# Kernel tuning notes

Measured on AMD Instinct MI355X. Metric: run time of the kernel, lower is better.

## Reference

```python
import jax, jax.numpy as jnp
import numpy as np

B, T, D, H, OUT = 1024, 512, 6, 128, 8


def setup_inputs() -> dict:
    key = jax.random.key(0)
    ks = jax.random.split(key, 24)
    n = lambda k, shp, s=0.05: jax.random.normal(k, shp, dtype=jnp.float32) * s
    return {
        "src": jax.random.normal(ks[0], (B, T, D), dtype=jnp.float32),
        # pointwise conv stack (kernel size 1 -> plain matmuls)
        "w0": n(ks[1], (H, D)), "b0": n(ks[2], (H,)),
        "w1": n(ks[3], (H, H)), "b1": n(ks[4], (H,)),
        "w2": n(ks[5], (H, H)), "b2": n(ks[6], (H,)),
        "w3": n(ks[7], (H, H)), "b3": n(ks[8], (H,)),
        "pos_embed": n(ks[9], (T, 1, H)),
        # LSTM layer 0 (PyTorch gate order i,f,g,o stacked along dim 0)
        "Wih0": n(ks[10], (4 * H, H)), "Whh0": n(ks[11], (4 * H, H)),
        "bih0": n(ks[12], (4 * H,)), "bhh0": n(ks[13], (4 * H,)),
        # LSTM layer 1
        "Wih1": n(ks[14], (4 * H, H)), "Whh1": n(ks[15], (4 * H, H)),
        "bih1": n(ks[16], (4 * H,)), "bhh1": n(ks[17], (4 * H,)),
        # head: LayerNorm + Linear(H, H//4) + GELU + Linear(H//4, OUT)
        "ln_g": jnp.ones((H,), jnp.float32), "ln_b": jnp.zeros((H,), jnp.float32),
        "hw1": n(ks[18], (H // 4, H)), "hb1": n(ks[19], (H // 4,)),
        "hw2": n(ks[20], (OUT, H // 4)), "hb2": n(ks[21], (OUT,)),
    }


def _gelu(x):
    return jax.nn.gelu(x, approximate=False)  # torch default GELU (erf)


def _lstm_layer(xs, Wih, Whh, bih, bhh):
    # xs: (T, B, H) time-major; returns (all hidden states, final hidden state)
    Hd = Whh.shape[1]
    Bd = xs.shape[1]
    bias = bih + bhh
    h0 = jnp.zeros((Bd, Hd), xs.dtype)
    c0 = jnp.zeros((Bd, Hd), xs.dtype)

    def step(carry, x):
        h, c = carry
        z = x @ Wih.T + h @ Whh.T + bias  # (B, 4H)
        i, f, g, o = jnp.split(z, 4, axis=-1)
        c = jax.nn.sigmoid(f) * c + jax.nn.sigmoid(i) * jnp.tanh(g)
        h = jax.nn.sigmoid(o) * jnp.tanh(c)
        return (h, c), h

    (h, _), ys = jax.lax.scan(step, (h0, c0), xs)
    return ys, h


def reference(src, w0, b0, w1, b1, w2, b2, w3, b3, pos_embed,
              Wih0, Whh0, bih0, bhh0, Wih1, Whh1, bih1, bhh1,
              ln_g, ln_b, hw1, hb1, hw2, hb2):
    # pointwise Conv1d+GELU stack (kernel=1 -> per-timestep matmul), eval mode
    x = _gelu(src @ w0.T + b0)            # (B, T, H)
    x = _gelu(x @ w1.T + b1)
    x = _gelu(x @ w2.T + b2)
    x = _gelu(x @ w3.T + b3)
    x = jnp.transpose(x, (1, 0, 2)) + pos_embed  # (T, B, H), broadcast pos over batch
    ys, _ = _lstm_layer(x, Wih0, Whh0, bih0, bhh0)
    _, h = _lstm_layer(ys, Wih1, Whh1, bih1, bhh1)  # final hidden of last layer, (B, H)
    # head: LayerNorm (eps=1e-5) -> Linear -> GELU -> Linear (dropout inactive in eval)
    mu = h.mean(-1, keepdims=True)
    var = ((h - mu) ** 2).mean(-1, keepdims=True)
    hn = (h - mu) * jax.lax.rsqrt(var + 1e-5) * ln_g + ln_b
    return _gelu(hn @ hw1.T + hb1) @ hw2.T + hb2  # (B, OUT)
```

## Files before the change

kernel.cpp:

```cpp
#include <hip/hip_runtime.h>
#include <hip/hip_bf16.h>
#include <cstdint>

#define T_ 512
#define B_ 1024
#define D_ 6
#define H_ 128
#define CH_ 8
#define CT_ 16

typedef _Float16 f16;
typedef _Float16 f16x8 __attribute__((ext_vector_type(8)));
typedef float f32x4 __attribute__((ext_vector_type(4)));

__device__ __forceinline__ float erf_f(float x) {
    float ax = fabsf(x);
    float t = __builtin_amdgcn_rcpf(fmaf(0.3275911f, ax, 1.f));
    float p = fmaf(t, 1.061405429f, -1.453152027f);
    p = fmaf(t, p, 1.421413741f);
    p = fmaf(t, p, -0.284496736f);
    p = fmaf(t, p, 0.254829592f);
    p = p * t;
    float e = __builtin_amdgcn_exp2f(-ax * ax * 1.4426950408889634f);
    float r = 1.f - p * e;
    return copysignf(r, x);
}
__device__ __forceinline__ float gelu_f(float x) {
    return 0.5f * x * (1.f + erf_f(x * 0.7071067811865476f));
}
__device__ __forceinline__ float sig_f(float x) {
    return __builtin_amdgcn_rcpf(1.f + __builtin_amdgcn_exp2f(-1.4426950408889634f * x));
}
__device__ __forceinline__ float tanh_f(float x) {
    return 2.f * sig_f(2.f * x) - 1.f;
}
__device__ __forceinline__ f16x8 load8cvt(const float* p) {
    float4 a = ((const float4*)p)[0];
    float4 b = ((const float4*)p)[1];
    f16x8 r = { (f16)a.x, (f16)a.y, (f16)a.z, (f16)a.w,
                (f16)b.x, (f16)b.y, (f16)b.z, (f16)b.w };
    return r;
}
__device__ __forceinline__ f16x8 lds_rd8(const f16* base, int row, int cb) {
    const char* p = (const char*)base + row * 256 + (cb ^ ((row & 7) << 4));
    return *(const f16x8*)p;
}
__device__ __forceinline__ void lds_wr1(f16* base, int row, int col, f16 v) {
    char* p = (char*)base + row * 256 + ((col * 2) ^ ((row & 7) << 4));
    *(f16*)p = v;
}
__device__ __forceinline__ void zx_wr(f16* base, int row, int col, f16 v) {
    char* p = (char*)base + row * 1024 + ((col * 2) ^ ((row & 7) << 4));
    *(f16*)p = v;
}
__device__ __forceinline__ float zx_rd(const f16* base, int row, int col) {
    const char* p = (const char*)base + row * 1024 + ((col * 2) ^ ((row & 7) << 4));
    return (float)*(const f16*)p;
}

__global__ __launch_bounds__(512) void conv_k(
    const float* __restrict__ src,
    const float* __restrict__ w0p, const float* __restrict__ b0p,
    const float* __restrict__ w1p, const float* __restrict__ b1p,
    const float* __restrict__ w2p, const float* __restrict__ b2p,
    const float* __restrict__ w3p, const float* __restrict__ b3p,
    const float* __restrict__ posp, f16* __restrict__ xout)
{
    __shared__ f16 XA0[64 * 128];
    __shared__ f16 XA1[64 * 128];
    const int tid = threadIdx.x;
    const int lane = tid & 63, wid = tid >> 6;
    const int l16 = lane & 15, hi = lane >> 4;
    const int t0 = (blockIdx.x & 31) * CT_;
    const int bb0 = (blockIdx.x >> 5) * 4;
    const int mycol = wid * 16 + l16;

    f16x8 cw[3][4];
    {
        const float* wp[3] = { w1p, w2p, w3p };
#pragma unroll
        for (int L = 0; L < 3; ++L)
#pragma unroll
            for (int ki = 0; ki < 4; ++ki)
                cw[L][ki] = load8cvt(wp[L] + mycol * 128 + ki * 32 + hi * 8);
    }
    const int col0 = tid & 127;
    const int r0 = tid >> 7;
    float w0c[6], b0c;
#pragma unroll
    for (int k = 0; k < 6; ++k) w0c[k] = w0p[col0 * 6 + k];
    b0c = b0p[col0];
    const float b1c = b1p[mycol], b2c = b2p[mycol], b3c = b3p[mycol];

    {
        const float2* sp0 = (const float2*)src + ((size_t)(bb0 + r0) * T_ + t0) * 3;
#pragma unroll
        for (int it = 0; it < CT_; ++it) {
            float2 a = sp0[it * 3 + 0], b = sp0[it * 3 + 1], c2 = sp0[it * 3 + 2];
            float acc = b0c;
            acc = fmaf(a.x, w0c[0], acc);
            acc = fmaf(a.y, w0c[1], acc);
            acc = fmaf(b.x, w0c[2], acc);
            acc = fmaf(b.y, w0c[3], acc);
            acc = fmaf(c2.x, w0c[4], acc);
            acc = fmaf(c2.y, w0c[5], acc);
            lds_wr1(XA0, it * 4 + r0, col0, (f16)gelu_f(acc));
        }
    }
    __syncthreads();

    auto conv_mfma = [&](const f16* Xin, f16* Xout, int L, float bc, bool addpos) {
#pragma unroll
        for (int mt = 0; mt < 4; ++mt) {
            f16x8 af[4];
#pragma unroll
            for (int ki = 0; ki < 4; ++ki)
                af[ki] = lds_rd8(Xin, mt * 16 + l16, ki * 64 + hi * 16);
            f32x4 acc = { bc, bc, bc, bc };
#pragma unroll
            for (int ki = 0; ki < 4; ++ki)
                acc = __builtin_amdgcn_mfma_f32_16x16x32_f16(af[ki], cw[L][ki], acc, 0, 0, 0);
            float pv = 0.f;
            if (addpos) pv = posp[(t0 + mt * 4 + hi) * 128 + mycol];
#pragma unroll
            for (int j = 0; j < 4; ++j)
                lds_wr1(Xout, mt * 16 + hi * 4 + j, mycol, (f16)(gelu_f(acc[j]) + pv));
        }
    };
    conv_mfma(XA0, XA1, 0, b1c, false);
    __syncthreads();
    conv_mfma(XA1, XA0, 1, b2c, false);
    __syncthreads();
    conv_mfma(XA0, XA1, 2, b3c, true);
    __syncthreads();

#pragma unroll
    for (int pass = 0; pass < 2; ++pass) {
        int u = pass * 512 + tid;
        int tau = u >> 4, cw8 = u & 15;
        f16x8 v = lds_rd8(XA1, tau, cw8 * 16);
        *(f16x8*)(xout + (size_t)(t0 + (tau >> 2)) * (B_ * H_) +
                  (size_t)(bb0 + (tau & 3)) * H_ + cw8 * 8) = v;
    }
}

template <bool WRITE_YS, bool WRITE_H>
__global__ __launch_bounds__(512) void lstm_chunk_k(
    const f16* __restrict__ xb,
    const float* __restrict__ Wih, const float* __restrict__ Whh,
    const float* __restrict__ bih, const float* __restrict__ bhh,
    f16* __restrict__ ys, float* __restrict__ hfin)
{
    __shared__ f16 ZX[32 * 512];
    __shared__ f16 YH[32 * 128];
    __shared__ f16 HL[2][4 * 128];

    const int tid = threadIdx.x;
    const int lane = tid & 63, wid = tid >> 6;
    const int l16 = lane & 15, hi = lane >> 4;
    const int bb0 = blockIdx.x * 4;
    const int mycol = wid * 16 + l16;

    f16x8 whh[4][4];
    float biasg[4];
#pragma unroll
    for (int g = 0; g < 4; ++g) {
        int n = g * 128 + mycol;
        biasg[g] = bih[n] + bhh[n];
#pragma unroll
        for (int ki = 0; ki < 4; ++ki)
            whh[g][ki] = load8cvt(Whh + n * 128 + ki * 32 + hi * 8);
    }
    for (int i = tid; i < 2 * 4 * 128; i += 512) ((f16*)HL)[i] = (f16)0.f;

    float c = 0.f, h = 0.f;
    __syncthreads();

    auto flushYH = [&](int tc) {
        int tau = tid >> 4, cw8 = tid & 15;
        f16x8 v = lds_rd8(YH, tau, cw8 * 16);
        *(f16x8*)(ys + (size_t)(tc + (tau >> 2)) * (B_ * H_) +
                  (size_t)(bb0 + (tau & 3)) * H_ + cw8 * 8) = v;
    };

    for (int t0 = 0; t0 < T_; t0 += CH_) {
        if (WRITE_YS && t0 > 0) flushYH(t0 - CH_);
        {
            f16x8 af[2][4];
#pragma unroll
            for (int mt = 0; mt < 2; ++mt) {
                const int tau = mt * 16 + l16;
                const f16* ap = xb + (size_t)(t0 + (tau >> 2)) * (B_ * H_) +
                                (size_t)(bb0 + (tau & 3)) * H_;
#pragma unroll
                for (int ki = 0; ki < 4; ++ki)
                    af[mt][ki] = *(const f16x8*)(ap + ki * 32 + hi * 8);
            }
#pragma unroll
            for (int nt = 0; nt < 4; ++nt) {
                const int n = wid * 64 + nt * 16 + l16;
                f16x8 bf[4];
#pragma unroll
                for (int ki = 0; ki < 4; ++ki)
                    bf[ki] = load8cvt(Wih + n * 128 + ki * 32 + hi * 8);
                f32x4 za0 = { 0.f, 0.f, 0.f, 0.f };
                f32x4 za1 = { 0.f, 0.f, 0.f, 0.f };
#pragma unroll
                for (int ki = 0; ki < 4; ++ki) {
                    za0 = __builtin_amdgcn_mfma_f32_16x16x32_f16(af[0][ki], bf[ki], za0, 0, 0, 0);
                    za1 = __builtin_amdgcn_mfma_f32_16x16x32_f16(af[1][ki], bf[ki], za1, 0, 0, 0);
                }
#pragma unroll
                for (int j = 0; j < 4; ++j) {
                    zx_wr(ZX, hi * 4 + j, wid * 64 + nt * 16 + l16, (f16)za0[j]);
                    zx_wr(ZX, 16 + hi * 4 + j, wid * 64 + nt * 16 + l16, (f16)za1[j]);
                }
                __builtin_amdgcn_sched_barrier(0);
            }
        }
        __syncthreads();
        for (int it = 0; it < CH_; ++it) {
            const int t = t0 + it;
            f16x8 ha[4];
#pragma unroll
            for (int ki = 0; ki < 4; ++ki)
                ha[ki] = lds_rd8(HL[t & 1], l16 >> 2, ki * 64 + hi * 16);
            f32x4 acc[4];
#pragma unroll
            for (int g = 0; g < 4; ++g) {
                f32x4 bv = { biasg[g], biasg[g], biasg[g], biasg[g] };
                acc[g] = bv;
            }
#pragma unroll
            for (int ki = 0; ki < 4; ++ki)
#pragma unroll
                for (int g = 0; g < 4; ++g)
                    acc[g] = __builtin_amdgcn_mfma_f32_16x16x32_f16(ha[ki], whh[g][ki], acc[g], 0, 0, 0);
            float zi = acc[0][0] + zx_rd(ZX, it * 4 + hi, 0 + mycol);
            float zf = acc[1][0] + zx_rd(ZX, it * 4 + hi, 128 + mycol);
            float zg = acc[2][0] + zx_rd(ZX, it * 4 + hi, 256 + mycol);
            float zo = acc[3][0] + zx_rd(ZX, it * 4 + hi, 384 + mycol);
            c = sig_f(zf) * c + sig_f(zi) * tanh_f(zg);
            h = sig_f(zo) * tanh_f(c);
            lds_wr1(HL[(t + 1) & 1], hi, mycol, (f16)h);
            if (WRITE_YS) lds_wr1(YH, it * 4 + hi, mycol, (f16)h);
            __syncthreads();
        }
    }
    if (WRITE_YS) flushYH(T_ - CH_);
    if (WRITE_H) hfin[(size_t)(bb0 + hi) * H_ + mycol] = h;
}

__global__ __launch_bounds__(256) void head_k(
    const float* __restrict__ hfin,
    const float* __restrict__ lng, const float* __restrict__ lnb,
    const float* __restrict__ hw1, const float* __restrict__ hb1,
    const float* __restrict__ hw2, const float* __restrict__ hb2,
    float* __restrict__ outp)
{
    __shared__ float HN[4][128];
    __shared__ float G[4][32];
    const int tid = threadIdx.x, lane = tid & 63, wid = tid >> 6;
    const int b = blockIdx.x * 4 + wid;
    float v0 = hfin[b * 128 + lane], v1 = hfin[b * 128 + 64 + lane];
    float s = v0 + v1;
#pragma unroll
    for (int m = 1; m < 64; m <<= 1) s += __shfl_xor(s, m);
    float mu = s * (1.f / 128.f);
    float d0 = v0 - mu, d1 = v1 - mu;
    float q = d0 * d0 + d1 * d1;
#pragma unroll
    for (int m = 1; m < 64; m <<= 1) q += __shfl_xor(q, m);
    float rs = rsqrtf(q * (1.f / 128.f) + 1e-5f);
    HN[wid][lane] = d0 * rs * lng[lane] + lnb[lane];
    HN[wid][64 + lane] = d1 * rs * lng[64 + lane] + lnb[64 + lane];
    __syncthreads();
    if (tid < 128) {
        int row = tid >> 5, o = tid & 31;
        float a = hb1[o];
#pragma unroll 4
        for (int k = 0; k < 128; ++k) a = fmaf(HN[row][k], hw1[o * 128 + k], a);
        G[row][o] = gelu_f(a);
    }
    __syncthreads();
    if (tid < 32) {
        int row = tid >> 3, oo = tid & 7;
        float a = hb2[oo];
#pragma unroll
        for (int k = 0; k < 32; ++k) a = fmaf(G[row][k], hw2[oo * 32 + k], a);
        outp[(size_t)(blockIdx.x * 4 + row) * 8 + oo] = a;
    }
}

extern "C" void kernel_launch(void* const* d_in, const int* in_sizes, int n_in,
                              void* d_out, int out_size, void* d_ws, size_t ws_size,
                              hipStream_t stream) {
    (void)in_sizes; (void)n_in; (void)out_size; (void)ws_size;
    const float* src  = (const float*)d_in[0];
    const float* w0   = (const float*)d_in[1];
    const float* b0   = (const float*)d_in[2];
    const float* w1   = (const float*)d_in[3];
    const float* b1   = (const float*)d_in[4];
    const float* w2   = (const float*)d_in[5];
    const float* b2   = (const float*)d_in[6];
    const float* w3   = (const float*)d_in[7];
    const float* b3   = (const float*)d_in[8];
    const float* pos  = (const float*)d_in[9];
    const float* Wih0 = (const float*)d_in[10];
    const float* Whh0 = (const float*)d_in[11];
    const float* bih0 = (const float*)d_in[12];
    const float* bhh0 = (const float*)d_in[13];
    const float* Wih1 = (const float*)d_in[14];
    const float* Whh1 = (const float*)d_in[15];
    const float* bih1 = (const float*)d_in[16];
    const float* bhh1 = (const float*)d_in[17];
    const float* lng  = (const float*)d_in[18];
    const float* lnb  = (const float*)d_in[19];
    const float* hw1  = (const float*)d_in[20];
    const float* hb1  = (const float*)d_in[21];
    const float* hw2  = (const float*)d_in[22];
    const float* hb2  = (const float*)d_in[23];
    float* outp = (float*)d_out;

    f16* xbuf = (f16*)d_ws;
    float* hfin = (float*)((char*)d_ws + (size_t)134217728);

    conv_k<<<dim3(8192), dim3(512), 0, stream>>>(
        src, w0, b0, w1, b1, w2, b2, w3, b3, pos, xbuf);
    lstm_chunk_k<true, false><<<dim3(256), dim3(512), 0, stream>>>(
        xbuf, Wih0, Whh0, bih0, bhh0, xbuf, nullptr);
    lstm_chunk_k<false, true><<<dim3(256), dim3(512), 0, stream>>>(
        xbuf, Wih1, Whh1, bih1, bhh1, nullptr, hfin);
    head_k<<<dim3(256), dim3(256), 0, stream>>>(
        hfin, lng, lnb, hw1, hb1, hw2, hb2, outp);
}
```

Before: 1.063 ms.

## Fuse both LSTM layers into one producer-consumer kernel with chunk flags

Replaces the two sequential LSTM layer launches with a single 512-block launch. The first 256 blocks run layer 0 and publish each finished 8-step chunk of hidden states through a per-batch-group release flag. The other 256 blocks spin on that flag and run layer 1 on each chunk as it arrives, so the two layers overlap in time instead of running back to back. The cost is extra fences and polling. It also relies on all 512 blocks being resident at once, and it can deadlock if a consumer block is scheduled while its producer block is not.

```diff
diff --git a/kernel.cpp b/kernel.cpp
--- a/kernel.cpp
+++ b/kernel.cpp
@@ -8,6 +8,7 @@
 #define H_ 128
 #define CH_ 8
 #define CT_ 16
+#define NP_ 256
 
 typedef _Float16 f16;
 typedef _Float16 f16x8 __attribute__((ext_vector_type(8)));
@@ -144,12 +145,14 @@
     }
 }
 
-template <bool WRITE_YS, bool WRITE_H>
-__global__ __launch_bounds__(512) void lstm_chunk_k(
+__global__ __launch_bounds__(512) void lstm_pc_k(
     const f16* __restrict__ xb,
-    const float* __restrict__ Wih, const float* __restrict__ Whh,
-    const float* __restrict__ bih, const float* __restrict__ bhh,
-    f16* __restrict__ ys, float* __restrict__ hfin)
+    const float* __restrict__ Wih0, const float* __restrict__ Whh0,
+    const float* __restrict__ bih0, const float* __restrict__ bhh0,
+    const float* __restrict__ Wih1, const float* __restrict__ Whh1,
+    const float* __restrict__ bih1, const float* __restrict__ bhh1,
+    f16* __restrict__ ys, int* __restrict__ flags,
+    float* __restrict__ hfin)
 {
     __shared__ f16 ZX[32 * 512];
     __shared__ f16 YH[32 * 128];
@@ -158,8 +161,15 @@
     const int tid = threadIdx.x;
     const int lane = tid & 63, wid = tid >> 6;
     const int l16 = lane & 15, hi = lane >> 4;
-    const int bb0 = blockIdx.x * 4;
+    const bool producer = (int)blockIdx.x < NP_;
+    const int p = producer ? (int)blockIdx.x : (int)blockIdx.x - NP_;
+    const int bb0 = p * 4;
     const int mycol = wid * 16 + l16;
+
+    const float* Wih = producer ? Wih0 : Wih1;
+    const float* Whh = producer ? Whh0 : Whh1;
+    const float* bih = producer ? bih0 : bih1;
+    const float* bhh = producer ? bhh0 : bhh1;
 
     f16x8 whh[4][4];
     float biasg[4];
@@ -176,49 +186,41 @@
     float c = 0.f, h = 0.f;
     __syncthreads();
 
-    auto flushYH = [&](int tc) {
-        int tau = tid >> 4, cw8 = tid & 15;
-        f16x8 v = lds_rd8(YH, tau, cw8 * 16);
-        *(f16x8*)(ys + (size_t)(tc + (tau >> 2)) * (B_ * H_) +
-                  (size_t)(bb0 + (tau & 3)) * H_ + cw8 * 8) = v;
+    auto zgemm = [&](const f16* Asrc , int t0) {
+        f16x8 af[2][4];
+#pragma unroll
+        for (int mt = 0; mt < 2; ++mt) {
+            const int tau = mt * 16 + l16;
+            const f16* ap = Asrc + (size_t)(t0 + (tau >> 2)) * (B_ * H_) +
+                            (size_t)(bb0 + (tau & 3)) * H_;
+#pragma unroll
+            for (int ki = 0; ki < 4; ++ki)
+                af[mt][ki] = *(const f16x8*)(ap + ki * 32 + hi * 8);
+        }
+#pragma unroll
+        for (int nt = 0; nt < 4; ++nt) {
+            const int n = wid * 64 + nt * 16 + l16;
+            f16x8 bf[4];
+#pragma unroll
+            for (int ki = 0; ki < 4; ++ki)
+                bf[ki] = load8cvt(Wih + n * 128 + ki * 32 + hi * 8);
+            f32x4 za0 = { 0.f, 0.f, 0.f, 0.f };
+            f32x4 za1 = { 0.f, 0.f, 0.f, 0.f };
+#pragma unroll
+            for (int ki = 0; ki < 4; ++ki) {
+                za0 = __builtin_amdgcn_mfma_f32_16x16x32_f16(af[0][ki], bf[ki], za0, 0, 0, 0);
+                za1 = __builtin_amdgcn_mfma_f32_16x16x32_f16(af[1][ki], bf[ki], za1, 0, 0, 0);
+            }
+#pragma unroll
+            for (int j = 0; j < 4; ++j) {
+                zx_wr(ZX, hi * 4 + j, wid * 64 + nt * 16 + l16, (f16)za0[j]);
+                zx_wr(ZX, 16 + hi * 4 + j, wid * 64 + nt * 16 + l16, (f16)za1[j]);
+            }
+            __builtin_amdgcn_sched_barrier(0);
+        }
     };
 
-    for (int t0 = 0; t0 < T_; t0 += CH_) {
-        if (WRITE_YS && t0 > 0) flushYH(t0 - CH_);
-        {
-            f16x8 af[2][4];
-#pragma unroll
-            for (int mt = 0; mt < 2; ++mt) {
-                const int tau = mt * 16 + l16;
-                const f16* ap = xb + (size_t)(t0 + (tau >> 2)) * (B_ * H_) +
-                                (size_t)(bb0 + (tau & 3)) * H_;
-#pragma unroll
-                for (int ki = 0; ki < 4; ++ki)
-                    af[mt][ki] = *(const f16x8*)(ap + ki * 32 + hi * 8);
-            }
-#pragma unroll
-            for (int nt = 0; nt < 4; ++nt) {
-                const int n = wid * 64 + nt * 16 + l16;
-                f16x8 bf[4];
-#pragma unroll
-                for (int ki = 0; ki < 4; ++ki)
-                    bf[ki] = load8cvt(Wih + n * 128 + ki * 32 + hi * 8);
-                f32x4 za0 = { 0.f, 0.f, 0.f, 0.f };
-                f32x4 za1 = { 0.f, 0.f, 0.f, 0.f };
-#pragma unroll
-                for (int ki = 0; ki < 4; ++ki) {
-                    za0 = __builtin_amdgcn_mfma_f32_16x16x32_f16(af[0][ki], bf[ki], za0, 0, 0, 0);
-                    za1 = __builtin_amdgcn_mfma_f32_16x16x32_f16(af[1][ki], bf[ki], za1, 0, 0, 0);
-                }
-#pragma unroll
-                for (int j = 0; j < 4; ++j) {
-                    zx_wr(ZX, hi * 4 + j, wid * 64 + nt * 16 + l16, (f16)za0[j]);
-                    zx_wr(ZX, 16 + hi * 4 + j, wid * 64 + nt * 16 + l16, (f16)za1[j]);
-                }
-                __builtin_amdgcn_sched_barrier(0);
-            }
-        }
-        __syncthreads();
+    auto slots = [&](int t0, bool writeYH) {
         for (int it = 0; it < CH_; ++it) {
             const int t = t0 + it;
             f16x8 ha[4];
@@ -243,12 +245,44 @@
             c = sig_f(zf) * c + sig_f(zi) * tanh_f(zg);
             h = sig_f(zo) * tanh_f(c);
             lds_wr1(HL[(t + 1) & 1], hi, mycol, (f16)h);
-            if (WRITE_YS) lds_wr1(YH, it * 4 + hi, mycol, (f16)h);
-            __syncthreads();
-        }
-    }
-    if (WRITE_YS) flushYH(T_ - CH_);
-    if (WRITE_H) hfin[(size_t)(bb0 + hi) * H_ + mycol] = h;
+            if (writeYH) lds_wr1(YH, it * 4 + hi, mycol, (f16)h);
+            __syncthreads();
+        }
+    };
+
+    if (producer) {
+        for (int k = 0; k < T_ / CH_; ++k) {
+            const int t0 = k * CH_;
+            zgemm(xb, t0);
+            __syncthreads();
+            slots(t0, true);
+            {
+                int tau = tid >> 4, cw8 = tid & 15;
+                f16x8 v = lds_rd8(YH, tau, cw8 * 16);
+                *(f16x8*)(ys + (size_t)(t0 + (tau >> 2)) * (B_ * H_) +
+                          (size_t)(bb0 + (tau & 3)) * H_ + cw8 * 8) = v;
+            }
+            __threadfence();
+            __syncthreads();
+            if (tid == 0)
+                __hip_atomic_store(&flags[p], k + 1, __ATOMIC_RELEASE,
+                                   __HIP_MEMORY_SCOPE_AGENT);
+        }
+    } else {
+        for (int k = 0; k < T_ / CH_; ++k) {
+            const int t0 = k * CH_;
+            if (tid == 0) {
+                while (__hip_atomic_load(&flags[p], __ATOMIC_ACQUIRE,
+                                         __HIP_MEMORY_SCOPE_AGENT) < k + 1)
+                    __builtin_amdgcn_s_sleep(8);
+            }
+            __syncthreads();
+            zgemm(ys, t0);
+            __syncthreads();
+            slots(t0, false);
+        }
+        hfin[(size_t)(bb0 + hi) * H_ + mycol] = h;
+    }
 }
 
 __global__ __launch_bounds__(256) void head_k(
@@ -324,13 +358,14 @@
 
     f16* xbuf = (f16*)d_ws;
     float* hfin = (float*)((char*)d_ws + (size_t)134217728);
-
+    int* flags = (int*)((char*)d_ws + (size_t)134742016);
+
+    hipMemsetAsync(flags, 0, 1024, stream);
     conv_k<<<dim3(8192), dim3(512), 0, stream>>>(
         src, w0, b0, w1, b1, w2, b2, w3, b3, pos, xbuf);
-    lstm_chunk_k<true, false><<<dim3(256), dim3(512), 0, stream>>>(
-        xbuf, Wih0, Whh0, bih0, bhh0, xbuf, nullptr);
-    lstm_chunk_k<false, true><<<dim3(256), dim3(512), 0, stream>>>(
-        xbuf, Wih1, Whh1, bih1, bhh1, nullptr, hfin);
+    lstm_pc_k<<<dim3(512), dim3(512), 0, stream>>>(
+        xbuf, Wih0, Whh0, bih0, bhh0, Wih1, Whh1, bih1, bhh1,
+        xbuf , flags, hfin);
     head_k<<<dim3(256), dim3(256), 0, stream>>>(
         hfin, lng, lnb, hw1, hb1, hw2, hb2, outp);
 }
```

Measured after the change: 3.609 ms. 3.4x slower.

## Double LSTM time chunk and pre-convert input weights to fp16

Applied to the files above, without the earlier changes.

The LSTM input projection now covers 16 timesteps per chunk instead of 8, so each fp16 Wih tile loaded from global memory feeds four MFMA row tiles instead of two, and the per-chunk barrier and projection overhead is amortised over more steps. A new prep kernel converts Wih0/Wih1 to fp16 once per call, removing the repeated fp32 load and convert in the loop. The pointer is laundered so the weight loads are not hoisted. The ZX and YH shared buffers double in size, which raises LDS use and register pressure and may cut occupancy.

```diff
diff --git a/kernel.cpp b/kernel.cpp
--- a/kernel.cpp
+++ b/kernel.cpp
@@ -6,7 +6,7 @@
 #define B_ 1024
 #define D_ 6
 #define H_ 128
-#define CH_ 8
+#define CH_ 16
 #define CT_ 16
 
 typedef _Float16 f16;
@@ -41,6 +41,10 @@
                 (f16)b.x, (f16)b.y, (f16)b.z, (f16)b.w };
     return r;
 }
+__device__ __forceinline__ const f16* launder16(const f16* p) {
+    asm volatile("" : "+s"(p));
+    return p;
+}
 __device__ __forceinline__ f16x8 lds_rd8(const f16* base, int row, int cb) {
     const char* p = (const char*)base + row * 256 + (cb ^ ((row & 7) << 4));
     return *(const f16x8*)p;
@@ -56,6 +60,15 @@
 __device__ __forceinline__ float zx_rd(const f16* base, int row, int col) {
     const char* p = (const char*)base + row * 1024 + ((col * 2) ^ ((row & 7) << 4));
     return (float)*(const f16*)p;
+}
+
+__global__ __launch_bounds__(512) void prep_k(
+    const float* __restrict__ Wih0, const float* __restrict__ Wih1,
+    f16* __restrict__ w0f, f16* __restrict__ w1f)
+{
+    int i = blockIdx.x * 512 + threadIdx.x;
+    w0f[i] = (f16)Wih0[i];
+    w1f[i] = (f16)Wih1[i];
 }
 
 __global__ __launch_bounds__(512) void conv_k(
@@ -147,12 +160,12 @@
 template <bool WRITE_YS, bool WRITE_H>
 __global__ __launch_bounds__(512) void lstm_chunk_k(
     const f16* __restrict__ xb,
-    const float* __restrict__ Wih, const float* __restrict__ Whh,
+    const f16* __restrict__ Wihf, const float* __restrict__ Whh,
     const float* __restrict__ bih, const float* __restrict__ bhh,
     f16* __restrict__ ys, float* __restrict__ hfin)
 {
-    __shared__ f16 ZX[32 * 512];
-    __shared__ f16 YH[32 * 128];
+    __shared__ f16 ZX[64 * 512];
+    __shared__ f16 YH[64 * 128];
     __shared__ f16 HL[2][4 * 128];
 
     const int tid = threadIdx.x;
@@ -177,18 +190,22 @@
     __syncthreads();
 
     auto flushYH = [&](int tc) {
-        int tau = tid >> 4, cw8 = tid & 15;
-        f16x8 v = lds_rd8(YH, tau, cw8 * 16);
-        *(f16x8*)(ys + (size_t)(tc + (tau >> 2)) * (B_ * H_) +
-                  (size_t)(bb0 + (tau & 3)) * H_ + cw8 * 8) = v;
+#pragma unroll
+        for (int pass = 0; pass < 2; ++pass) {
+            int u = pass * 512 + tid;
+            int tau = u >> 4, cw8 = u & 15;
+            f16x8 v = lds_rd8(YH, tau, cw8 * 16);
+            *(f16x8*)(ys + (size_t)(tc + (tau >> 2)) * (B_ * H_) +
+                      (size_t)(bb0 + (tau & 3)) * H_ + cw8 * 8) = v;
+        }
     };
 
     for (int t0 = 0; t0 < T_; t0 += CH_) {
         if (WRITE_YS && t0 > 0) flushYH(t0 - CH_);
         {
-            f16x8 af[2][4];
-#pragma unroll
-            for (int mt = 0; mt < 2; ++mt) {
+            f16x8 af[4][4];
+#pragma unroll
+            for (int mt = 0; mt < 4; ++mt) {
                 const int tau = mt * 16 + l16;
                 const f16* ap = xb + (size_t)(t0 + (tau >> 2)) * (B_ * H_) +
                                 (size_t)(bb0 + (tau & 3)) * H_;
@@ -196,25 +213,31 @@
                 for (int ki = 0; ki < 4; ++ki)
                     af[mt][ki] = *(const f16x8*)(ap + ki * 32 + hi * 8);
             }
+            const f16* Wf = launder16(Wihf);
 #pragma unroll
             for (int nt = 0; nt < 4; ++nt) {
                 const int n = wid * 64 + nt * 16 + l16;
                 f16x8 bf[4];
 #pragma unroll
                 for (int ki = 0; ki < 4; ++ki)
-                    bf[ki] = load8cvt(Wih + n * 128 + ki * 32 + hi * 8);
-                f32x4 za0 = { 0.f, 0.f, 0.f, 0.f };
-                f32x4 za1 = { 0.f, 0.f, 0.f, 0.f };
-#pragma unroll
-                for (int ki = 0; ki < 4; ++ki) {
-                    za0 = __builtin_amdgcn_mfma_f32_16x16x32_f16(af[0][ki], bf[ki], za0, 0, 0, 0);
-                    za1 = __builtin_amdgcn_mfma_f32_16x16x32_f16(af[1][ki], bf[ki], za1, 0, 0, 0);
+                    bf[ki] = *(const f16x8*)(Wf + n * 128 + ki * 32 + hi * 8);
+                f32x4 za[4];
+#pragma unroll
+                for (int mt = 0; mt < 4; ++mt) {
+                    f32x4 zz = { 0.f, 0.f, 0.f, 0.f };
+                    za[mt] = zz;
                 }
 #pragma unroll
-                for (int j = 0; j < 4; ++j) {
-                    zx_wr(ZX, hi * 4 + j, wid * 64 + nt * 16 + l16, (f16)za0[j]);
-                    zx_wr(ZX, 16 + hi * 4 + j, wid * 64 + nt * 16 + l16, (f16)za1[j]);
-                }
+                for (int ki = 0; ki < 4; ++ki)
+#pragma unroll
+                    for (int mt = 0; mt < 4; ++mt)
+                        za[mt] = __builtin_amdgcn_mfma_f32_16x16x32_f16(
+                            af[mt][ki], bf[ki], za[mt], 0, 0, 0);
+#pragma unroll
+                for (int mt = 0; mt < 4; ++mt)
+#pragma unroll
+                    for (int j = 0; j < 4; ++j)
+                        zx_wr(ZX, mt * 16 + hi * 4 + j, n, (f16)za[mt][j]);
                 __builtin_amdgcn_sched_barrier(0);
             }
         }
@@ -324,13 +347,16 @@
 
     f16* xbuf = (f16*)d_ws;
     float* hfin = (float*)((char*)d_ws + (size_t)134217728);
-
+    f16* w0f = (f16*)((char*)d_ws + (size_t)134742016);
+    f16* w1f = (f16*)((char*)d_ws + (size_t)134873088);
+
+    prep_k<<<dim3(128), dim3(512), 0, stream>>>(Wih0, Wih1, w0f, w1f);
     conv_k<<<dim3(8192), dim3(512), 0, stream>>>(
         src, w0, b0, w1, b1, w2, b2, w3, b3, pos, xbuf);
     lstm_chunk_k<true, false><<<dim3(256), dim3(512), 0, stream>>>(
-        xbuf, Wih0, Whh0, bih0, bhh0, xbuf, nullptr);
+        xbuf, w0f, Whh0, bih0, bhh0, xbuf, nullptr);
     lstm_chunk_k<false, true><<<dim3(256), dim3(512), 0, stream>>>(
-        xbuf, Wih1, Whh1, bih1, bhh1, nullptr, hfin);
+        xbuf, w1f, Whh1, bih1, bhh1, nullptr, hfin);
     head_k<<<dim3(256), dim3(256), 0, stream>>>(
         hfin, lng, lnb, hw1, hb1, hw2, hb2, outp);
 }
```

New measurement: 1.280 ms. 20.4% more time.
